# Performance work log

Hardware: AMD Instinct MI355X
Metric: run time of the kernel (lower is better)

The kernel has to match this reference:

```python
import jax, jax.numpy as jnp
import numpy as np

DIM = 512
HEADS = 8
HEAD_DIM = DIM // HEADS
EPS = 1e-5

def _ln(x, g, b):
    m = jnp.mean(x, axis=-1, keepdims=True)
    v = jnp.mean((x - m) ** 2, axis=-1, keepdims=True)
    return (x - m) * jax.lax.rsqrt(v + EPS) * g + b

def setup_inputs() -> dict:
    key = jax.random.key(0)
    ks = jax.random.split(key, 12)
    s = 0.02
    d, dff = DIM, 4 * DIM
    inp = {
        'x': jax.random.normal(ks[0], (8, 4096, d), jnp.float32),
        'Wq': jax.random.normal(ks[1], (d, d), jnp.float32) * s,
        'bq': jnp.zeros((d,), jnp.float32),
        'Wk': jax.random.normal(ks[2], (d, d), jnp.float32) * s,
        'bk': jnp.zeros((d,), jnp.float32),
        'Wv': jax.random.normal(ks[3], (d, d), jnp.float32) * s,
        'bv': jnp.zeros((d,), jnp.float32),
        'Wo': jax.random.normal(ks[4], (d, d), jnp.float32) * s,
        'bo': jnp.zeros((d,), jnp.float32),
        'g1': jnp.ones((d,), jnp.float32),
        'b1': jnp.zeros((d,), jnp.float32),
        'g2': jnp.ones((d,), jnp.float32),
        'b2': jnp.zeros((d,), jnp.float32),
        'Wf1': jax.random.normal(ks[5], (d, dff), jnp.float32) * s,
        'bf1': jnp.zeros((dff,), jnp.float32),
        'Wf2': jax.random.normal(ks[6], (dff, d), jnp.float32) * s,
        'bf2': jnp.zeros((d,), jnp.float32),
    }
    return inp

def _linear_attn(x, Wq, bq, Wk, bk, Wv, bv, Wo, bo):
    b, n, d = x.shape
    def split(t):
        return t.reshape(b, n, HEADS, HEAD_DIM).transpose(0, 2, 1, 3)  # bhnd
    q = split(x @ Wq + bq)
    k = split(x @ Wk + bk)
    v = split(x @ Wv + bv)
    q = jax.nn.elu(q) + 1.0
    k = jax.nn.elu(k) + 1.0
    kv = jnp.einsum('bhnd,bhnf->bhdf', k, v)
    out = jnp.einsum('bhnd,bhdf->bhnf', q, kv)
    out = out.transpose(0, 2, 1, 3).reshape(b, n, d)
    return out @ Wo + bo

def reference(x, Wq, bq, Wk, bk, Wv, bv, Wo, bo, g1, b1, g2, b2, Wf1, bf1, Wf2, bf2):
    # series decomposition: AvgPool1d(k=3, stride=1, pad=1, count_include_pad=True)
    xp = jnp.pad(x, ((0, 0), (1, 1), (0, 0)))
    trend = (xp[:, :-2] + xp[:, 1:-1] + xp[:, 2:]) / 3.0
    seasonal = x - trend
    seasonal = seasonal + _linear_attn(_ln(seasonal, g1, b1), Wq, bq, Wk, bk, Wv, bv, Wo, bo)
    h = _ln(seasonal, g2, b2)
    h = jax.nn.gelu(h @ Wf1 + bf1, approximate=False) @ Wf2 + bf2
    seasonal = seasonal + h
    return seasonal + trend
```

## Files before the change

kernel.cpp:

```cpp
#include <hip/hip_runtime.h>
#include <math.h>

typedef __bf16 bf16;
typedef __attribute__((ext_vector_type(8))) __bf16 bf16x8;
typedef __attribute__((ext_vector_type(4))) float floatx4;

#define DIM 512
#define DFF 2048
#define SEQ 4096
#define ROWS 32768

#define GLOBAL_AS(p) ((const __attribute__((address_space(1))) void*)(p))
#define LDS_AS(p)    ((__attribute__((address_space(3))) void*)(p))

__global__ __launch_bounds__(256) void prep_w_kernel(const float* __restrict__ W,
                                                     bf16* __restrict__ Wt, int K, int N)
{
    int idx = blockIdx.x * 256 + threadIdx.x;
    if (idx >= K * N) return;
    int k = idx % K;
    int n = idx / K;
    Wt[idx] = (bf16)W[(size_t)k * N + n];
}

__global__ __launch_bounds__(256) void prep_w3_kernel(const float* __restrict__ Wq,
                                                      const float* __restrict__ Wk,
                                                      const float* __restrict__ Wv,
                                                      bf16* __restrict__ Wt)
{
    int idx = blockIdx.x * 256 + threadIdx.x;
    int which = idx >> 18;
    int r = idx & 262143;
    int k = r & 511;
    int n = r >> 9;
    const float* W = (which == 0) ? Wq : (which == 1 ? Wk : Wv);
    Wt[idx] = (bf16)W[(size_t)k * 512 + n];
}

__global__ __launch_bounds__(256) void pack_bias_kernel(const float* __restrict__ bq,
                                                        const float* __restrict__ bk,
                                                        const float* __restrict__ bv,
                                                        float* __restrict__ out)
{
    int i = blockIdx.x * 256 + threadIdx.x;
    if (i >= 1536) return;
    out[i] = (i < 512) ? bq[i] : (i < 1024 ? bk[i - 512] : bv[i - 1024]);
}

__device__ inline float wave_red(float v)
{
#pragma unroll
    for (int off = 32; off; off >>= 1) v += __shfl_xor(v, off, 64);
    return v;
}

__global__ __launch_bounds__(256) void decomp_ln_kernel(const float* __restrict__ x,
                                                        const float* __restrict__ g,
                                                        const float* __restrict__ be,
                                                        float* __restrict__ S,
                                                        bf16* __restrict__ XN)
{
    int wave = threadIdx.x >> 6, lane = threadIdx.x & 63;
    int r = blockIdx.x * 4 + wave;
    int n = r & (SEQ - 1);
    const float4* xr = (const float4*)(x + (size_t)r * DIM);
    float4 z = make_float4(0.f, 0.f, 0.f, 0.f);
    float s[8];
#pragma unroll
    for (int i = 0; i < 2; ++i) {
        int c4 = lane * 2 + i;
        float4 v0 = xr[c4];
        float4 vm = (n > 0)       ? xr[c4 - DIM / 4] : z;
        float4 vp = (n < SEQ - 1) ? xr[c4 + DIM / 4] : z;
        s[i * 4 + 0] = v0.x - (vm.x + v0.x + vp.x) * (1.f / 3.f);
        s[i * 4 + 1] = v0.y - (vm.y + v0.y + vp.y) * (1.f / 3.f);
        s[i * 4 + 2] = v0.z - (vm.z + v0.z + vp.z) * (1.f / 3.f);
        s[i * 4 + 3] = v0.w - (vm.w + v0.w + vp.w) * (1.f / 3.f);
    }
    float4* Sr = (float4*)(S + (size_t)r * DIM);
    Sr[lane * 2]     = make_float4(s[0], s[1], s[2], s[3]);
    Sr[lane * 2 + 1] = make_float4(s[4], s[5], s[6], s[7]);

    float sum = 0.f;
#pragma unroll
    for (int j = 0; j < 8; ++j) sum += s[j];
    sum = wave_red(sum);
    float mean = sum * (1.f / DIM);
    float vs = 0.f;
#pragma unroll
    for (int j = 0; j < 8; ++j) { float d = s[j] - mean; vs += d * d; }
    vs = wave_red(vs);
    float rstd = rsqrtf(vs * (1.f / DIM) + 1e-5f);

    int c = lane * 8;
    float4 g0 = ((const float4*)(g + c))[0],  g1v = ((const float4*)(g + c))[1];
    float4 b0 = ((const float4*)(be + c))[0], b1v = ((const float4*)(be + c))[1];
    bf16x8 o;
    o[0] = (bf16)((s[0] - mean) * rstd * g0.x + b0.x);
    o[1] = (bf16)((s[1] - mean) * rstd * g0.y + b0.y);
    o[2] = (bf16)((s[2] - mean) * rstd * g0.z + b0.z);
    o[3] = (bf16)((s[3] - mean) * rstd * g0.w + b0.w);
    o[4] = (bf16)((s[4] - mean) * rstd * g1v.x + b1v.x);
    o[5] = (bf16)((s[5] - mean) * rstd * g1v.y + b1v.y);
    o[6] = (bf16)((s[6] - mean) * rstd * g1v.z + b1v.z);
    o[7] = (bf16)((s[7] - mean) * rstd * g1v.w + b1v.w);
    *(bf16x8*)(XN + (size_t)r * DIM + c) = o;
}

__global__ __launch_bounds__(256) void ln_kernel(const float* __restrict__ X,
                                                 const float* __restrict__ g,
                                                 const float* __restrict__ be,
                                                 bf16* __restrict__ XN)
{
    int wave = threadIdx.x >> 6, lane = threadIdx.x & 63;
    int r = blockIdx.x * 4 + wave;
    const float4* xr = (const float4*)(X + (size_t)r * DIM);
    float4 a0 = xr[lane * 2], a1 = xr[lane * 2 + 1];
    float s[8] = {a0.x, a0.y, a0.z, a0.w, a1.x, a1.y, a1.z, a1.w};
    float sum = 0.f;
#pragma unroll
    for (int j = 0; j < 8; ++j) sum += s[j];
    sum = wave_red(sum);
    float mean = sum * (1.f / DIM);
    float vs = 0.f;
#pragma unroll
    for (int j = 0; j < 8; ++j) { float d = s[j] - mean; vs += d * d; }
    vs = wave_red(vs);
    float rstd = rsqrtf(vs * (1.f / DIM) + 1e-5f);
    int c = lane * 8;
    float4 g0 = ((const float4*)(g + c))[0],  g1v = ((const float4*)(g + c))[1];
    float4 b0 = ((const float4*)(be + c))[0], b1v = ((const float4*)(be + c))[1];
    bf16x8 o;
    o[0] = (bf16)((s[0] - mean) * rstd * g0.x + b0.x);
    o[1] = (bf16)((s[1] - mean) * rstd * g0.y + b0.y);
    o[2] = (bf16)((s[2] - mean) * rstd * g0.z + b0.z);
    o[3] = (bf16)((s[3] - mean) * rstd * g0.w + b0.w);
    o[4] = (bf16)((s[4] - mean) * rstd * g1v.x + b1v.x);
    o[5] = (bf16)((s[5] - mean) * rstd * g1v.y + b1v.y);
    o[6] = (bf16)((s[6] - mean) * rstd * g1v.z + b1v.z);
    o[7] = (bf16)((s[7] - mean) * rstd * g1v.w + b1v.w);
    *(bf16x8*)(XN + (size_t)r * DIM + c) = o;
}

enum { M_QKV = 0, M_ATTN = 1, M_FFN1 = 2, M_FFN2 = 3 };

template <int MODE>
__global__ __launch_bounds__(256) void gemm_bt_kernel(const bf16* __restrict__ A, int lda,
                                                      const bf16* __restrict__ Bt,
                                                      const float* __restrict__ bias,
                                                      float* S, const float* __restrict__ X,
                                                      void* Cout, int ldc,
                                                      int N, int K, int rows_per_batch,
                                                      int m_off)
{
    __shared__ __align__(16) bf16 lA[3][128 * 32];
    __shared__ __align__(16) bf16 lB[3][128 * 32];
    int tid = threadIdx.x;

    int nwg = gridDim.x * gridDim.y;
    int orig = blockIdx.y * gridDim.x + blockIdx.x;
    int wg = (orig & 7) * (nwg >> 3) + (orig >> 3);
    int m0 = (wg / gridDim.x) * 128;
    int n0 = (wg % gridDim.x) * 128;

    const bf16* Abase = A + (size_t)m0 * lda;
    const bf16* Bbase = Bt + (size_t)n0 * K;
    if (rows_per_batch) Bbase += (size_t)(m0 / rows_per_batch) * (size_t)N * K;

    int lane = tid & 63;
    int wave = tid >> 6;
    int wm = (wave >> 1) * 64;
    int wn = (wave & 1) * 64;
    int lm = lane & 15;
    int quad = lane >> 4;
    int i0w = tid & 192;

    floatx4 acc[4][4];
#pragma unroll
    for (int i = 0; i < 4; ++i)
#pragma unroll
        for (int j = 0; j < 4; ++j) acc[i][j] = (floatx4){0.f, 0.f, 0.f, 0.f};

    auto stage = [&](int buf, int k0) {
#pragma unroll
        for (int it = 0; it < 2; ++it) {
            int ib = it * 256 + i0w;
            int i  = ib + lane;
            int row = i >> 2;
            int col = ((i & 3) ^ (row & 3)) * 8;
            __builtin_amdgcn_global_load_lds(GLOBAL_AS(Abase + (size_t)row * lda + k0 + col),
                                             LDS_AS(&lA[buf][ib * 8]), 16, 0, 0);
            __builtin_amdgcn_global_load_lds(GLOBAL_AS(Bbase + (size_t)row * K + k0 + col),
                                             LDS_AS(&lB[buf][ib * 8]), 16, 0, 0);
        }
    };

    stage(0, 0);
    stage(1, 32);
    asm volatile("s_waitcnt vmcnt(4)" ::: "memory");
    __builtin_amdgcn_s_barrier();

    int nsteps = K >> 5;
    int cur = 0;
    for (int s = 0; s < nsteps; ++s) {
        bf16x8 af[4], bfv[4];
#pragma unroll
        for (int i = 0; i < 4; ++i) {
            int ra = wm + i * 16 + lm;
            af[i] = *(const bf16x8*)&lA[cur][ra * 32 + (quad ^ (ra & 3)) * 8];
        }
#pragma unroll
        for (int j = 0; j < 4; ++j) {
            int rb = wn + j * 16 + lm;
            bfv[j] = *(const bf16x8*)&lB[cur][rb * 32 + (quad ^ (rb & 3)) * 8];
        }

        int kpre = (s + 2) << 5;
        bool issued = kpre < K;
        if (issued) {
            int nxt = cur + 2; if (nxt >= 3) nxt -= 3;
            stage(nxt, kpre);
        }

#pragma unroll
        for (int i = 0; i < 4; ++i)
#pragma unroll
            for (int j = 0; j < 4; ++j)
                acc[i][j] = __builtin_amdgcn_mfma_f32_16x16x32_bf16(af[i], bfv[j], acc[i][j], 0, 0, 0);

        if (issued) asm volatile("s_waitcnt vmcnt(4)" ::: "memory");
        else        asm volatile("s_waitcnt vmcnt(0)" ::: "memory");
        __builtin_amdgcn_s_barrier();
        cur = (cur == 2) ? 0 : cur + 1;
    }

#pragma unroll
    for (int i = 0; i < 4; ++i) {
        int gm_base = m0 + wm + i * 16 + quad * 4;
#pragma unroll
        for (int j = 0; j < 4; ++j) {
            int gn = n0 + wn + j * 16 + lm;
            float bia = bias[gn];
            if constexpr (MODE == M_FFN2) {
                int gmg0 = m_off + gm_base;
                int bn = gmg0 & (SEQ - 1);
                size_t ob = (size_t)gmg0 * DIM + gn;
                const float* Xb = X + ob;
                float xr6[6];
#pragma unroll
                for (int r = 0; r < 6; ++r) {
                    int nr = bn + r - 1;
                    xr6[r] = (nr >= 0 && nr < SEQ) ? Xb[(long)(r - 1) * DIM] : 0.f;
                }
                float* op = (float*)Cout;
#pragma unroll
                for (int e = 0; e < 4; ++e) {
                    size_t o = ob + (size_t)e * DIM;
                    float val = acc[i][j][e] + bia;
                    op[o] = val + op[o] + (xr6[e] + xr6[e + 1] + xr6[e + 2]) * (1.f / 3.f);
                }
            } else {
#pragma unroll
                for (int e = 0; e < 4; ++e) {
                    int gm = gm_base + e;
                    float val = acc[i][j][e] + bia;
                    if constexpr (MODE == M_QKV) {
                        if (gn < 1024) val = (val > 0.f) ? val + 1.f : __expf(val);
                        ((bf16*)Cout)[(size_t)gm * ldc + gn] = (bf16)val;
                    } else if constexpr (MODE == M_ATTN) {
                        S[(size_t)gm * DIM + gn] += val;
                    } else {
                        val = 0.5f * val * (1.f + erff(val * 0.70710678118654752f));
                        ((bf16*)Cout)[(size_t)gm * ldc + gn] = (bf16)val;
                    }
                }
            }
        }
    }
}

__global__ __launch_bounds__(256) void kv_mfma_kernel(const bf16* __restrict__ QKV,
                                                      float* __restrict__ KV)
{
    int kc = blockIdx.x, h = blockIdx.y, b = blockIdx.z;
    __shared__ __align__(16) bf16 lbuf[3][2 * 128 * 64];
    int tid = threadIdx.x;
    int lane = tid & 63, wave = tid >> 6;
    int lm = lane & 15, quad = lane >> 4;

    floatx4 acc[4][4];
#pragma unroll
    for (int i = 0; i < 4; ++i)
#pragma unroll
        for (int j = 0; j < 4; ++j) acc[i][j] = (floatx4){0.f, 0.f, 0.f, 0.f};

    const bf16* kb = QKV + (size_t)b * SEQ * 1536 + 512 + (size_t)h * 64;
    const bf16* vb = kb + 512;
    int drow = lane >> 3;
    int d0 = (lane & 7) * 8;

    auto stage = [&](int buf, int it) {
        int n0 = kc * 1024 + it * 128;
#pragma unroll
        for (int q = 0; q < 4; ++q) {
            int nbase = wave * 32 + q * 8;
            int ldsoff = wave * 2048 + q * 512;
            __builtin_amdgcn_global_load_lds(GLOBAL_AS(kb + (size_t)(n0 + nbase + drow) * 1536 + d0),
                                             LDS_AS(&lbuf[buf][ldsoff]), 16, 0, 0);
            __builtin_amdgcn_global_load_lds(GLOBAL_AS(vb + (size_t)(n0 + nbase + drow) * 1536 + d0),
                                             LDS_AS(&lbuf[buf][8192 + ldsoff]), 16, 0, 0);
        }
    };

    stage(0, 0);
    stage(1, 1);
    asm volatile("s_waitcnt vmcnt(8)" ::: "memory");
    __builtin_amdgcn_s_barrier();

    int cur = 0;
    for (int it = 0; it < 8; ++it) {
        const bf16* lk = lbuf[cur];
        const bf16* lv = lbuf[cur] + 8192;
        int nw = wave * 32 + quad * 8;
        bf16x8 af[4], bfv[4];
#pragma unroll
        for (int i = 0; i < 4; ++i) {
            int dd = i * 16 + lm;
#pragma unroll
            for (int j = 0; j < 8; ++j) af[i][j] = lk[(nw + j) * 64 + dd];
#pragma unroll
            for (int j = 0; j < 8; ++j) bfv[i][j] = lv[(nw + j) * 64 + dd];
        }

        bool issued = (it + 2) < 8;
        if (issued) {
            int nxt = cur + 2; if (nxt >= 3) nxt -= 3;
            stage(nxt, it + 2);
        }

#pragma unroll
        for (int i = 0; i < 4; ++i)
#pragma unroll
            for (int j = 0; j < 4; ++j)
                acc[i][j] = __builtin_amdgcn_mfma_f32_16x16x32_bf16(af[i], bfv[j], acc[i][j], 0, 0, 0);

        if (issued) asm volatile("s_waitcnt vmcnt(8)" ::: "memory");
        else        asm volatile("s_waitcnt vmcnt(0)" ::: "memory");
        __builtin_amdgcn_s_barrier();
        cur = (cur == 2) ? 0 : cur + 1;
    }

    __syncthreads();
    float* red = (float*)lbuf;
    if (wave < 2) {
#pragma unroll
        for (int i = 0; i < 4; ++i)
#pragma unroll
            for (int j = 0; j < 4; ++j)
#pragma unroll
                for (int e = 0; e < 4; ++e)
                    red[wave * 4096 + (i * 16 + quad * 4 + e) * 64 + j * 16 + lm] = acc[i][j][e];
    }
    __syncthreads();
    if (wave >= 2) {
#pragma unroll
        for (int i = 0; i < 4; ++i)
#pragma unroll
            for (int j = 0; j < 4; ++j)
#pragma unroll
                for (int e = 0; e < 4; ++e)
                    red[(wave - 2) * 4096 + (i * 16 + quad * 4 + e) * 64 + j * 16 + lm] += acc[i][j][e];
    }
    __syncthreads();
    float* dst = KV + ((size_t)kc * 64 + b * 8 + h) * 4096;
#pragma unroll
    for (int p = 0; p < 4; ++p) {
        int e4 = (tid + p * 256) * 4;
        float4 a = *(const float4*)&red[e4];
        float4 c4 = *(const float4*)&red[4096 + e4];
        a.x += c4.x; a.y += c4.y; a.z += c4.z; a.w += c4.w;
        *(float4*)&dst[e4] = a;
    }
}

__global__ __launch_bounds__(256) void kvw_kernel(const float* __restrict__ KV,
                                                  const float* __restrict__ Wo,
                                                  bf16* __restrict__ KVWT)
{
    int jc = blockIdx.x & 7, bh = blockIdx.x >> 3;
    int h = bh & 7, b = bh >> 3;
    __shared__ float skvT[64 * 68];
    int tid = threadIdx.x;
    const float* src = KV + (size_t)bh * 4096;
#pragma unroll
    for (int p = 0; p < 16; ++p) {
        int e = tid + p * 256;
        float s = src[e] + src[e + 262144] + src[e + 524288] + src[e + 786432];
        skvT[(e & 63) * 68 + (e >> 6)] = s;
    }
    __syncthreads();

    int j = tid & 63, dq = tid >> 6;
    int j0 = jc * 64;
    floatx4 acc4[4];
#pragma unroll
    for (int c = 0; c < 4; ++c) acc4[c] = (floatx4){0.f, 0.f, 0.f, 0.f};
    const float* wop = Wo + (size_t)h * 64 * 512 + j0 + j;
#pragma unroll 8
    for (int f = 0; f < 64; ++f) {
        float w = wop[(size_t)f * 512];
        const float* sp = &skvT[f * 68 + dq * 16];
#pragma unroll
        for (int c = 0; c < 4; ++c) {
            floatx4 s = *(const floatx4*)(sp + c * 4);
            acc4[c] += s * w;
        }
    }
    bf16* dst = KVWT + (size_t)b * 262144 + (size_t)(j0 + j) * 512 + h * 64 + dq * 16;
    bf16x8 o0, o1;
#pragma unroll
    for (int t = 0; t < 8; ++t) { o0[t] = (bf16)acc4[t >> 2][t & 3]; o1[t] = (bf16)acc4[2 + (t >> 2)][t & 3]; }
    *(bf16x8*)dst = o0;
    *(bf16x8*)(dst + 8) = o1;
}

extern "C" void kernel_launch(void* const* d_in, const int* in_sizes, int n_in,
                              void* d_out, int out_size, void* d_ws, size_t ws_size,
                              hipStream_t stream)
{
    const float* x   = (const float*)d_in[0];
    const float* Wq  = (const float*)d_in[1];
    const float* bq  = (const float*)d_in[2];
    const float* Wk  = (const float*)d_in[3];
    const float* bk  = (const float*)d_in[4];
    const float* Wv  = (const float*)d_in[5];
    const float* bv  = (const float*)d_in[6];
    const float* Wo  = (const float*)d_in[7];
    const float* bo  = (const float*)d_in[8];
    const float* g1  = (const float*)d_in[9];
    const float* b1  = (const float*)d_in[10];
    const float* g2  = (const float*)d_in[11];
    const float* b2  = (const float*)d_in[12];
    const float* Wf1 = (const float*)d_in[13];
    const float* bf1 = (const float*)d_in[14];
    const float* Wf2 = (const float*)d_in[15];
    const float* bf2 = (const float*)d_in[16];
    float* out = (float*)d_out;
    (void)in_sizes; (void)n_in; (void)out_size;

    char* ws = (char*)d_ws;
    size_t off = 0;
    auto alloc = [&](size_t bytes) -> char* {
        char* p = ws + off;
        off += (bytes + 255) & ~(size_t)255;
        return p;
    };
    bf16*  WqkvT = (bf16*)alloc((size_t)1536 * 512 * 2);
    float* bias3 = (float*)alloc(1536 * 4);
    bf16*  Wf1T  = (bf16*)alloc((size_t)2048 * 512 * 2);
    bf16*  Wf2T  = (bf16*)alloc((size_t)512 * 2048 * 2);
    size_t post_xn_off = 0;
    bf16*  XN    = (bf16*)alloc((size_t)ROWS * DIM * 2);
    post_xn_off = off;
    float* KV    = (float*)alloc((size_t)4 * 64 * 4096 * 4);
    bf16*  KVWT  = (bf16*)alloc((size_t)8 * 512 * 512 * 2);
    bf16*  QKV   = (bf16*)alloc((size_t)ROWS * 1536 * 2);

    size_t h1_bytes  = (size_t)ROWS * DFF * 2;
    bool   merged    = ws_size >= post_xn_off + h1_bytes;
    bf16*  H1full    = (bf16*)(ws + post_xn_off);
    bf16*  H1chunk   = QKV;

    prep_w3_kernel<<<3072, 256, 0, stream>>>(Wq, Wk, Wv, WqkvT);
    prep_w_kernel<<<4096, 256, 0, stream>>>(Wf1, Wf1T, 512, 2048);
    prep_w_kernel<<<4096, 256, 0, stream>>>(Wf2, Wf2T, 2048, 512);
    pack_bias_kernel<<<6, 256, 0, stream>>>(bq, bk, bv, bias3);

    decomp_ln_kernel<<<8192, 256, 0, stream>>>(x, g1, b1, out, XN);

    gemm_bt_kernel<M_QKV><<<dim3(12, 256), 256, 0, stream>>>(
        XN, 512, WqkvT, bias3, nullptr, nullptr, QKV, 1536, 1536, 512, 0, 0);

    kv_mfma_kernel<<<dim3(4, 8, 8), 256, 0, stream>>>(QKV, KV);

    kvw_kernel<<<512, 256, 0, stream>>>(KV, Wo, KVWT);

    gemm_bt_kernel<M_ATTN><<<dim3(4, 256), 256, 0, stream>>>(
        QKV, 1536, KVWT, bo, out, nullptr, nullptr, 0, 512, 512, 4096, 0);

    ln_kernel<<<8192, 256, 0, stream>>>(out, g2, b2, XN);

    if (merged) {
        gemm_bt_kernel<M_FFN1><<<dim3(16, 256), 256, 0, stream>>>(
            XN, 512, Wf1T, bf1, nullptr, nullptr, H1full, 2048, 2048, 512, 0, 0);
        gemm_bt_kernel<M_FFN2><<<dim3(4, 256), 256, 0, stream>>>(
            H1full, 2048, Wf2T, bf2, nullptr, x, out, 512, 512, 2048, 0, 0);
    } else {
        for (int c = 0; c < 2; ++c) {
            gemm_bt_kernel<M_FFN1><<<dim3(16, 128), 256, 0, stream>>>(
                XN + (size_t)c * 16384 * 512, 512, Wf1T, bf1, nullptr, nullptr,
                H1chunk, 2048, 2048, 512, 0, 0);
            gemm_bt_kernel<M_FFN2><<<dim3(4, 128), 256, 0, stream>>>(
                H1chunk, 2048, Wf2T, bf2, nullptr, x, out, 512, 512, 2048, 0, c * 16384);
        }
    }
}
```

Measured before the change: 629.4 us.

## Enlarge GEMM tiles to 256x128 with 512 threads and 64-deep K steps

The shared bf16 GEMM kernel now uses 256x128 output tiles computed by 8 waves (512 threads) instead of 128x128 by 4 waves. Each pipeline step now covers 64 of K instead of 32, using triple-buffered LDS with an 8-way XOR swizzle. MFMA blocks are wrapped in s_setprio to favour the math waves. All launch grids are halved in the M dimension to match. The aim is more data reuse per loaded tile and fewer barriers per unit of K. The cost is about 147KB of LDS per block, which allows only one block per CU and may reduce latency hiding.

```diff
diff --git a/kernel.cpp b/kernel.cpp
--- a/kernel.cpp
+++ b/kernel.cpp
@@ -145,22 +145,22 @@
 enum { M_QKV = 0, M_ATTN = 1, M_FFN1 = 2, M_FFN2 = 3 };
 
 template <int MODE>
-__global__ __launch_bounds__(256) void gemm_bt_kernel(const bf16* __restrict__ A, int lda,
-                                                      const bf16* __restrict__ Bt,
-                                                      const float* __restrict__ bias,
-                                                      float* S, const float* __restrict__ X,
-                                                      void* Cout, int ldc,
-                                                      int N, int K, int rows_per_batch,
-                                                      int m_off)
-{
-    __shared__ __align__(16) bf16 lA[3][128 * 32];
-    __shared__ __align__(16) bf16 lB[3][128 * 32];
+__global__ __launch_bounds__(512, 2) void gemm_bt_kernel(const bf16* __restrict__ A, int lda,
+                                                         const bf16* __restrict__ Bt,
+                                                         const float* __restrict__ bias,
+                                                         float* S, const float* __restrict__ X,
+                                                         void* Cout, int ldc,
+                                                         int N, int K, int rows_per_batch,
+                                                         int m_off)
+{
+    __shared__ __align__(16) bf16 lA0[256 * 64], lA1[256 * 64], lA2[256 * 64];
+    __shared__ __align__(16) bf16 lB0[128 * 64], lB1[128 * 64], lB2[128 * 64];
     int tid = threadIdx.x;
 
     int nwg = gridDim.x * gridDim.y;
     int orig = blockIdx.y * gridDim.x + blockIdx.x;
     int wg = (orig & 7) * (nwg >> 3) + (orig >> 3);
-    int m0 = (wg / gridDim.x) * 128;
+    int m0 = (wg / gridDim.x) * 256;
     int n0 = (wg % gridDim.x) * 128;
 
     const bf16* Abase = A + (size_t)m0 * lda;
@@ -173,7 +173,7 @@
     int wn = (wave & 1) * 64;
     int lm = lane & 15;
     int quad = lane >> 4;
-    int i0w = tid & 192;
+    int ebase = tid & 448;
 
     floatx4 acc[4][4];
 #pragma unroll
@@ -181,57 +181,65 @@
 #pragma unroll
         for (int j = 0; j < 4; ++j) acc[i][j] = (floatx4){0.f, 0.f, 0.f, 0.f};
 
-    auto stage = [&](int buf, int k0) {
-#pragma unroll
-        for (int it = 0; it < 2; ++it) {
-            int ib = it * 256 + i0w;
-            int i  = ib + lane;
-            int row = i >> 2;
-            int col = ((i & 3) ^ (row & 3)) * 8;
+    auto stage = [&](bf16* __restrict__ dA, bf16* __restrict__ dB, int k0) {
+#pragma unroll
+        for (int l = 0; l < 4; ++l) {
+            int e  = l * 512 + tid;
+            int eb = l * 512 + ebase;
+            int row = e >> 3;
+            int col = ((e & 7) ^ (row & 7)) * 8;
             __builtin_amdgcn_global_load_lds(GLOBAL_AS(Abase + (size_t)row * lda + k0 + col),
-                                             LDS_AS(&lA[buf][ib * 8]), 16, 0, 0);
-            __builtin_amdgcn_global_load_lds(GLOBAL_AS(Bbase + (size_t)row * K + k0 + col),
-                                             LDS_AS(&lB[buf][ib * 8]), 16, 0, 0);
+                                             LDS_AS(dA + eb * 8), 16, 0, 0);
+            if (l < 2)
+                __builtin_amdgcn_global_load_lds(GLOBAL_AS(Bbase + (size_t)row * K + k0 + col),
+                                                 LDS_AS(dB + eb * 8), 16, 0, 0);
         }
     };
 
-    stage(0, 0);
-    stage(1, 32);
-    asm volatile("s_waitcnt vmcnt(4)" ::: "memory");
-    __builtin_amdgcn_s_barrier();
-
-    int nsteps = K >> 5;
-    int cur = 0;
-    for (int s = 0; s < nsteps; ++s) {
-        bf16x8 af[4], bfv[4];
+    auto phase = [&](const bf16* cA, const bf16* cB, bf16* sA, bf16* sB, int knext) {
+        bf16x8 a0[4], a1[4], b0[4], b1[4];
 #pragma unroll
         for (int i = 0; i < 4; ++i) {
             int ra = wm + i * 16 + lm;
-            af[i] = *(const bf16x8*)&lA[cur][ra * 32 + (quad ^ (ra & 3)) * 8];
+            a0[i] = *(const bf16x8*)&cA[ra * 64 + ((quad     ^ (ra & 7)) * 8)];
+            a1[i] = *(const bf16x8*)&cA[ra * 64 + (((4 + quad) ^ (ra & 7)) * 8)];
         }
 #pragma unroll
         for (int j = 0; j < 4; ++j) {
             int rb = wn + j * 16 + lm;
-            bfv[j] = *(const bf16x8*)&lB[cur][rb * 32 + (quad ^ (rb & 3)) * 8];
-        }
-
-        int kpre = (s + 2) << 5;
-        bool issued = kpre < K;
-        if (issued) {
-            int nxt = cur + 2; if (nxt >= 3) nxt -= 3;
-            stage(nxt, kpre);
-        }
-
+            b0[j] = *(const bf16x8*)&cB[rb * 64 + ((quad     ^ (rb & 7)) * 8)];
+            b1[j] = *(const bf16x8*)&cB[rb * 64 + (((4 + quad) ^ (rb & 7)) * 8)];
+        }
+        bool issued = knext < K;
+        if (issued) stage(sA, sB, knext);
+        __builtin_amdgcn_s_setprio(1);
 #pragma unroll
         for (int i = 0; i < 4; ++i)
 #pragma unroll
             for (int j = 0; j < 4; ++j)
-                acc[i][j] = __builtin_amdgcn_mfma_f32_16x16x32_bf16(af[i], bfv[j], acc[i][j], 0, 0, 0);
-
-        if (issued) asm volatile("s_waitcnt vmcnt(4)" ::: "memory");
+                acc[i][j] = __builtin_amdgcn_mfma_f32_16x16x32_bf16(a0[i], b0[j], acc[i][j], 0, 0, 0);
+#pragma unroll
+        for (int i = 0; i < 4; ++i)
+#pragma unroll
+            for (int j = 0; j < 4; ++j)
+                acc[i][j] = __builtin_amdgcn_mfma_f32_16x16x32_bf16(a1[i], b1[j], acc[i][j], 0, 0, 0);
+        __builtin_amdgcn_s_setprio(0);
+        if (issued) asm volatile("s_waitcnt vmcnt(6)" ::: "memory");
         else        asm volatile("s_waitcnt vmcnt(0)" ::: "memory");
         __builtin_amdgcn_s_barrier();
-        cur = (cur == 2) ? 0 : cur + 1;
+    };
+
+    stage(lA0, lB0, 0);
+    stage(lA1, lB1, 64);
+    asm volatile("s_waitcnt vmcnt(6)" ::: "memory");
+    __builtin_amdgcn_s_barrier();
+
+    int nsteps = K >> 6;
+    int s = 0;
+    while (s < nsteps) {
+        phase(lA0, lB0, lA2, lB2, (s + 2) << 6); ++s; if (s >= nsteps) break;
+        phase(lA1, lB1, lA0, lB0, (s + 2) << 6); ++s; if (s >= nsteps) break;
+        phase(lA2, lB2, lA1, lB1, (s + 2) << 6); ++s;
     }
 
 #pragma unroll
@@ -478,29 +486,29 @@
 
     decomp_ln_kernel<<<8192, 256, 0, stream>>>(x, g1, b1, out, XN);
 
-    gemm_bt_kernel<M_QKV><<<dim3(12, 256), 256, 0, stream>>>(
+    gemm_bt_kernel<M_QKV><<<dim3(12, 128), 512, 0, stream>>>(
         XN, 512, WqkvT, bias3, nullptr, nullptr, QKV, 1536, 1536, 512, 0, 0);
 
     kv_mfma_kernel<<<dim3(4, 8, 8), 256, 0, stream>>>(QKV, KV);
 
     kvw_kernel<<<512, 256, 0, stream>>>(KV, Wo, KVWT);
 
-    gemm_bt_kernel<M_ATTN><<<dim3(4, 256), 256, 0, stream>>>(
+    gemm_bt_kernel<M_ATTN><<<dim3(4, 128), 512, 0, stream>>>(
         QKV, 1536, KVWT, bo, out, nullptr, nullptr, 0, 512, 512, 4096, 0);
 
     ln_kernel<<<8192, 256, 0, stream>>>(out, g2, b2, XN);
 
     if (merged) {
-        gemm_bt_kernel<M_FFN1><<<dim3(16, 256), 256, 0, stream>>>(
+        gemm_bt_kernel<M_FFN1><<<dim3(16, 128), 512, 0, stream>>>(
             XN, 512, Wf1T, bf1, nullptr, nullptr, H1full, 2048, 2048, 512, 0, 0);
-        gemm_bt_kernel<M_FFN2><<<dim3(4, 256), 256, 0, stream>>>(
+        gemm_bt_kernel<M_FFN2><<<dim3(4, 128), 512, 0, stream>>>(
             H1full, 2048, Wf2T, bf2, nullptr, x, out, 512, 512, 2048, 0, 0);
     } else {
         for (int c = 0; c < 2; ++c) {
-            gemm_bt_kernel<M_FFN1><<<dim3(16, 128), 256, 0, stream>>>(
+            gemm_bt_kernel<M_FFN1><<<dim3(16, 64), 512, 0, stream>>>(
                 XN + (size_t)c * 16384 * 512, 512, Wf1T, bf1, nullptr, nullptr,
                 H1chunk, 2048, 2048, 512, 0, 0);
-            gemm_bt_kernel<M_FFN2><<<dim3(4, 128), 256, 0, stream>>>(
+            gemm_bt_kernel<M_FFN2><<<dim3(4, 64), 512, 0, stream>>>(
                 H1chunk, 2048, Wf2T, bf2, nullptr, x, out, 512, 512, 2048, 0, c * 16384);
         }
     }
```

Measured after the change: 733.7 us. 16.6% more time.
